# Performance work log

Hardware: AMD Instinct MI355X
Metric: run time of the kernel (lower is better)

Reference implementation:

```python
import jax, jax.numpy as jnp
import numpy as np

N = 50000        # nodes
E = 1_600_000    # edges
IN = 64          # in_feats
H = 128          # h_feats
L = 5            # num_layers
G = 512          # graphs in batch
C = 10           # num_classes


def setup_inputs() -> dict:
    key = jax.random.key(0)
    ks = jax.random.split(key, 12)
    s = 0.05
    x = jax.random.normal(ks[0], (N, IN), jnp.float32)
    edge_index = jax.random.randint(ks[1], (2, E), 0, N, dtype=jnp.int32)
    batch = jnp.sort(jax.random.randint(ks[2], (N,), 0, G, dtype=jnp.int32))
    edge_weight = jax.random.uniform(ks[3], (E,), jnp.float32)
    # GatedGraphConv params: per-layer mixing weight + shared GRUCell
    weight = jax.random.normal(ks[4], (L, H, H), jnp.float32) * s
    w_ih = jax.random.normal(ks[5], (3 * H, H), jnp.float32) * s
    w_hh = jax.random.normal(ks[6], (3 * H, H), jnp.float32) * s
    b_ih = jax.random.normal(ks[7], (3 * H,), jnp.float32) * s
    b_hh = jax.random.normal(ks[8], (3 * H,), jnp.float32) * s
    # MLP head
    dense1_w = jax.random.normal(ks[9], (4 * H, H), jnp.float32) * s
    dense1_b = jnp.zeros((4 * H,), jnp.float32)
    dense2_w = jax.random.normal(ks[10], (C, 4 * H), jnp.float32) * s
    dense2_b = jnp.zeros((C,), jnp.float32)
    return dict(x=x, edge_index=edge_index, batch=batch, edge_weight=edge_weight,
                weight=weight, w_ih=w_ih, w_hh=w_hh, b_ih=b_ih, b_hh=b_hh,
                dense1_w=dense1_w, dense1_b=dense1_b,
                dense2_w=dense2_w, dense2_b=dense2_b)


def _gru_cell(m, h, w_ih, w_hh, b_ih, b_hh):
    # torch.nn.GRUCell(input=m, hidden=h)
    gi = m @ w_ih.T + b_ih
    gh = h @ w_hh.T + b_hh
    i_r, i_z, i_n = jnp.split(gi, 3, axis=-1)
    h_r, h_z, h_n = jnp.split(gh, 3, axis=-1)
    r = jax.nn.sigmoid(i_r + h_r)
    z = jax.nn.sigmoid(i_z + h_z)
    n = jnp.tanh(i_n + r * h_n)
    return (1.0 - z) * n + z * h


def reference(x, edge_index, batch, edge_weight, weight, w_ih, w_hh, b_ih, b_hh,
              dense1_w, dense1_b, dense2_w, dense2_b):
    src, dst = edge_index[0], edge_index[1]
    # pad in_feats -> h_feats (PyG GatedGraphConv)
    h = jnp.pad(x, ((0, 0), (0, H - IN)))
    for l in range(L):
        m = h @ weight[l]                          # [N, H]
        msg = m[src] * edge_weight[:, None]        # gather + edge gating [E, H]
        agg = jax.ops.segment_sum(msg, dst, num_segments=N)  # scatter-add
        h = _gru_cell(agg, h, w_ih, w_hh, b_ih, b_hh)
    pooled = jax.ops.segment_max(h, batch, num_segments=G)   # global max pool [G, H]
    # dropout is identity in eval mode
    hid = jax.nn.relu(pooled @ dense1_w.T + dense1_b)
    out = hid @ dense2_w.T + dense2_b
    return out
```

## Files before the change

### kernel.cpp

```cpp
#include <hip/hip_runtime.h>
#include <hip/hip_bf16.h>

#define NN 50000
#define NE 1600000
#define FIN 64
#define H 128
#define NL 5
#define NG 512
#define NC 10

typedef __attribute__((ext_vector_type(8))) short short8;
typedef __attribute__((ext_vector_type(4))) float f32x4;

#define OFF_H2A   0
#define OFF_H2B   3200000
#define OFF_CUR   6400000
#define OFF_OFF   6450176
#define OFF_CSR   6500352
#define OFF_POOL  8900352
#define OFF_FWF   8965888
#define OFF_FWHH  9088768

__device__ __forceinline__ short rne_bf16(float f){
    unsigned u = __float_as_uint(f);
    unsigned r = (u + 0x7FFFu + ((u >> 16) & 1u)) >> 16;
    return (short)r;
}
__device__ __forceinline__ float bf_lo(unsigned v){ return __uint_as_float(v << 16); }
__device__ __forceinline__ float bf_hi(unsigned v){ return __uint_as_float(v & 0xFFFF0000u); }


__global__ void k_hist(const int* __restrict__ ei, int* __restrict__ cnt){
    int e = blockIdx.x*256 + threadIdx.x;
    if (e < NE) atomicAdd(&cnt[ei[NE + e]], 1);
}

__global__ void k_scan(int* __restrict__ cur, int* __restrict__ off){
    __shared__ int s[1024];
    int t = threadIdx.x;
    const int CH = 49;
    int base = t*CH;
    int m = (NN + 1) - base; if (m > CH) m = CH; if (m < 0) m = 0;
    int sum = 0;
    for (int i = 0; i < m; ++i) sum += (cur[base + i] + 15) & ~15;
    s[t] = sum; __syncthreads();
    for (int o = 1; o < 1024; o <<= 1){
        int v = (t >= o) ? s[t - o] : 0; __syncthreads();
        s[t] += v; __syncthreads();
    }
    int run = s[t] - sum;
    for (int i = 0; i < m; ++i){
        int c = (cur[base + i] + 15) & ~15;
        off[base + i] = run;
        cur[base + i] = run;
        run += c;
    }
}

__global__ void k_fill(const int* __restrict__ ei, const float* __restrict__ ew,
                       int* __restrict__ cur, unsigned* __restrict__ csr){
    int e = blockIdx.x*256 + threadIdx.x;
    if (e >= NE) return;
    int src = ei[e], dst = ei[NE + e];
    int pos = atomicAdd(&cur[dst], 1);
    csr[pos] = (unsigned)src | (((unsigned)(ushort)rne_bf16(ew[e])) << 16);
}


__global__ void k_pad(const float* __restrict__ x, ushort* __restrict__ h2a){
    int idx = blockIdx.x*256 + threadIdx.x;
    int n = idx >> 7, f = idx & 127;
    float v = (f < FIN) ? x[n*FIN + f] : 0.f;
    h2a[idx] = (ushort)rne_bf16(v);
}

__global__ void k_fuse(const float* __restrict__ W, const float* __restrict__ wih,
                       short* __restrict__ fwf){
    int idx = blockIdx.x*256 + threadIdx.x;
    int l = idx / 49152;
    int r = idx % 49152;
    int k = r / 384, n = r % 384;
    const float* wl = W + l*16384 + k*128;
    const float* wi = wih + n*128;
    float acc = 0.f;
    for (int c = 0; c < 128; ++c) acc += wl[c]*wi[c];
    int lane = ((k>>3)&3)*16 + (n&15);
    fwf[l*49152 + (((n>>4)*4 + (k>>5))*64 + lane)*8 + (k&7)] = rne_bf16(acc);
}

__global__ void k_cvt_whh(const float* __restrict__ whh, short* __restrict__ fwhh){
    int idx = blockIdx.x*256 + threadIdx.x;
    int k = idx / 384, n = idx % 384;
    float v = whh[n*128 + k];
    int lane = ((k>>3)&3)*16 + (n&15);
    fwhh[(((n>>4)*4 + (k>>5))*64 + lane)*8 + (k&7)] = rne_bf16(v);
}

__global__ void k_init_pool(unsigned* __restrict__ p){
    p[blockIdx.x*256 + threadIdx.x] = 0x007FFFFFu;
}

__global__ __launch_bounds__(256)
void k_layer(const ushort* __restrict__ h2r, ushort* __restrict__ h2w,
             const int* __restrict__ off, const unsigned* __restrict__ csr,
             const short* __restrict__ fwf, const short* __restrict__ fwhh,
             const float* __restrict__ b_ih, const float* __restrict__ b_hh,
             const int* __restrict__ batch, unsigned* __restrict__ pooled,
             int last){
    __shared__ ushort tl[16*136];
    int tid = threadIdx.x;
    int n0 = blockIdx.x * 16;
    int wave = tid >> 6, lane = tid & 63;
    int lane_lo = lane & 15, quad = lane >> 4;
    int grp = lane >> 4, fl = lane & 15;

    for (int sub = 0; sub < 4; ++sub){
        int node = n0 + wave*4 + sub;
        int start = __builtin_amdgcn_readfirstlane(off[node]);
        int end   = __builtin_amdgcn_readfirstlane(off[node + 1]);
        float a0=0.f,a1=0.f,a2=0.f,a3=0.f,a4=0.f,a5=0.f,a6=0.f,a7=0.f;
        const ushort* hb = h2r + fl*8;
        for (int i = start; i < end; i += 16){
            uint4 c = *(const uint4*)(csr + i + grp*4);
            uint4 v0 = *(const uint4*)(hb + (c.x & 0xFFFFu)*H);
            uint4 v1 = *(const uint4*)(hb + (c.y & 0xFFFFu)*H);
            uint4 v2 = *(const uint4*)(hb + (c.z & 0xFFFFu)*H);
            uint4 v3 = *(const uint4*)(hb + (c.w & 0xFFFFu)*H);
            float w0 = bf_hi(c.x), w1 = bf_hi(c.y), w2 = bf_hi(c.z), w3 = bf_hi(c.w);
            a0 += w0*bf_lo(v0.x); a1 += w0*bf_hi(v0.x); a2 += w0*bf_lo(v0.y); a3 += w0*bf_hi(v0.y);
            a4 += w0*bf_lo(v0.z); a5 += w0*bf_hi(v0.z); a6 += w0*bf_lo(v0.w); a7 += w0*bf_hi(v0.w);
            a0 += w1*bf_lo(v1.x); a1 += w1*bf_hi(v1.x); a2 += w1*bf_lo(v1.y); a3 += w1*bf_hi(v1.y);
            a4 += w1*bf_lo(v1.z); a5 += w1*bf_hi(v1.z); a6 += w1*bf_lo(v1.w); a7 += w1*bf_hi(v1.w);
            a0 += w2*bf_lo(v2.x); a1 += w2*bf_hi(v2.x); a2 += w2*bf_lo(v2.y); a3 += w2*bf_hi(v2.y);
            a4 += w2*bf_lo(v2.z); a5 += w2*bf_hi(v2.z); a6 += w2*bf_lo(v2.w); a7 += w2*bf_hi(v2.w);
            a0 += w3*bf_lo(v3.x); a1 += w3*bf_hi(v3.x); a2 += w3*bf_lo(v3.y); a3 += w3*bf_hi(v3.y);
            a4 += w3*bf_lo(v3.z); a5 += w3*bf_hi(v3.z); a6 += w3*bf_lo(v3.w); a7 += w3*bf_hi(v3.w);
        }
        a0 += __shfl_xor(a0,16); a1 += __shfl_xor(a1,16); a2 += __shfl_xor(a2,16); a3 += __shfl_xor(a3,16);
        a4 += __shfl_xor(a4,16); a5 += __shfl_xor(a5,16); a6 += __shfl_xor(a6,16); a7 += __shfl_xor(a7,16);
        a0 += __shfl_xor(a0,32); a1 += __shfl_xor(a1,32); a2 += __shfl_xor(a2,32); a3 += __shfl_xor(a3,32);
        a4 += __shfl_xor(a4,32); a5 += __shfl_xor(a5,32); a6 += __shfl_xor(a6,32); a7 += __shfl_xor(a7,32);
        if (lane < 16){
            short8 hbv;
            hbv[0]=rne_bf16(a0); hbv[1]=rne_bf16(a1); hbv[2]=rne_bf16(a2); hbv[3]=rne_bf16(a3);
            hbv[4]=rne_bf16(a4); hbv[5]=rne_bf16(a5); hbv[6]=rne_bf16(a6); hbv[7]=rne_bf16(a7);
            *(short8*)(tl + (wave*4 + sub)*136 + fl*8) = hbv;
        }
    }
    __syncthreads();

    f32x4 ai[6], ah[6];
    #pragma unroll
    for (int i = 0; i < 6; ++i){ ai[i] = (f32x4){0.f,0.f,0.f,0.f}; ah[i] = (f32x4){0.f,0.f,0.f,0.f}; }

    const ushort* arow_t = tl + lane_lo*136;
    const ushort* arow_h = h2r + (size_t)(n0 + lane_lo)*H;
    #pragma unroll
    for (int kt = 0; kt < 4; ++kt){
        short8 at  = *(const short8*)(arow_t + kt*32 + quad*8);
        short8 ahh = *(const short8*)(arow_h + kt*32 + quad*8);
        #pragma unroll
        for (int s = 0; s < 3; ++s){
            #pragma unroll
            for (int t16 = 0; t16 < 2; ++t16){
                int tile = (s*8 + wave*2 + t16)*4 + kt;
                short8 bi = *(const short8*)(fwf  + tile*512 + lane*8);
                short8 bh = *(const short8*)(fwhh + tile*512 + lane*8);
                ai[s*2+t16] = __builtin_amdgcn_mfma_f32_16x16x32_bf16(at,  bi, ai[s*2+t16], 0, 0, 0);
                ah[s*2+t16] = __builtin_amdgcn_mfma_f32_16x16x32_bf16(ahh, bh, ah[s*2+t16], 0, 0, 0);
            }
        }
    }

    #pragma unroll
    for (int t16 = 0; t16 < 2; ++t16){
        int j = wave*32 + t16*16 + lane_lo;
        float bir = b_ih[j], biz = b_ih[128 + j], bin_ = b_ih[256 + j];
        float bhr = b_hh[j], bhz = b_hh[128 + j], bhn  = b_hh[256 + j];
        #pragma unroll
        for (int r = 0; r < 4; ++r){
            int row = n0 + quad*4 + r;
            float gir = ai[t16][r]     + bir, ghr = ah[t16][r]     + bhr;
            float giz = ai[2 + t16][r] + biz, ghz = ah[2 + t16][r] + bhz;
            float gin = ai[4 + t16][r] + bin_, ghn = ah[4 + t16][r] + bhn;
            float rr = 1.f/(1.f + __expf(-(gir + ghr)));
            float zz = 1.f/(1.f + __expf(-(giz + ghz)));
            float nn = tanhf(gin + rr*ghn);
            float ho = __uint_as_float(((unsigned)h2r[(size_t)row*H + j]) << 16);
            float hv = (1.f - zz)*nn + zz*ho;
            if (!last){
                h2w[(size_t)row*H + j] = (ushort)rne_bf16(hv);
            } else {
                int g = batch[row];
                unsigned u = __float_as_uint(hv);
                u = (u & 0x80000000u) ? ~u : (u | 0x80000000u);
                atomicMax(pooled + g*H + j, u);
            }
        }
    }
}


__global__ void k_head(const unsigned* __restrict__ pooled,
                       const float* __restrict__ d1w, const float* __restrict__ d1b,
                       const float* __restrict__ d2w, const float* __restrict__ d2b,
                       float* __restrict__ out){
    __shared__ float sp[128];
    __shared__ float shid[512];
    int g = blockIdx.x, tid = threadIdx.x;
    if (tid < 128){
        unsigned u = pooled[g*H + tid];
        sp[tid] = __uint_as_float((u & 0x80000000u) ? (u ^ 0x80000000u) : ~u);
    }
    __syncthreads();
    for (int o = tid; o < 512; o += 256){
        float acc = d1b[o];
        for (int k = 0; k < H; ++k) acc += sp[k] * d1w[o*H + k];
        shid[o] = fmaxf(acc, 0.f);
    }
    __syncthreads();
    if (tid < NC){
        float acc = d2b[tid];
        for (int o = 0; o < 512; ++o) acc += shid[o] * d2w[tid*512 + o];
        out[g*NC + tid] = acc;
    }
}

extern "C" void kernel_launch(void* const* d_in, const int* in_sizes, int n_in,
                              void* d_out, int out_size, void* d_ws, size_t ws_size,
                              hipStream_t stream){
    const float* x     = (const float*)d_in[0];
    const int*   ei    = (const int*)d_in[1];
    const int*   batch = (const int*)d_in[2];
    const float* ew    = (const float*)d_in[3];
    const float* W     = (const float*)d_in[4];
    const float* wih   = (const float*)d_in[5];
    const float* whh   = (const float*)d_in[6];
    const float* bih   = (const float*)d_in[7];
    const float* bhh   = (const float*)d_in[8];
    const float* d1w   = (const float*)d_in[9];
    const float* d1b   = (const float*)d_in[10];
    const float* d2w   = (const float*)d_in[11];
    const float* d2b   = (const float*)d_in[12];
    float* out = (float*)d_out;

    float*  ws  = (float*)d_ws;
    ushort* h2a = (ushort*)(ws + OFF_H2A);
    ushort* h2b = (ushort*)(ws + OFF_H2B);
    int*    cur = (int*)(ws + OFF_CUR);
    int*    off = (int*)(ws + OFF_OFF);
    unsigned* csr = (unsigned*)(ws + OFF_CSR);
    unsigned* pooled = (unsigned*)(ws + OFF_POOL);
    short*  fwf  = (short*)(ws + OFF_FWF);
    short*  fwhh = (short*)(ws + OFF_FWHH);

    hipMemsetAsync(cur, 0, 50176*sizeof(int), stream);
    hipMemsetAsync(csr, 0, 2400000*sizeof(unsigned), stream);
    k_hist<<<6250, 256, 0, stream>>>(ei, cur);
    k_scan<<<1, 1024, 0, stream>>>(cur, off);
    k_fill<<<6250, 256, 0, stream>>>(ei, ew, cur, csr);

    k_fuse<<<960, 256, 0, stream>>>(W, wih, fwf);
    k_cvt_whh<<<192, 256, 0, stream>>>(whh, fwhh);
    k_pad<<<25000, 256, 0, stream>>>(x, h2a);
    k_init_pool<<<256, 256, 0, stream>>>(pooled);

    for (int l = 0; l < NL; ++l){
        ushort* h2r = (l & 1) ? h2b : h2a;
        ushort* h2w = (l & 1) ? h2a : h2b;
        k_layer<<<3125, 256, 0, stream>>>(h2r, h2w, off, csr,
                                          fwf + (size_t)l*49152, fwhh, bih, bhh,
                                          batch, pooled, (l == NL-1) ? 1 : 0);
    }

    k_head<<<NG, 256, 0, stream>>>(pooled, d1w, d1b, d2w, d2b, out);
}
```

Baseline: 920.5 us.

## Renumber nodes by descending in-degree to balance per-block gather work

```diff
diff --git a/kernel.cpp b/kernel.cpp
--- a/kernel.cpp
+++ b/kernel.cpp
@@ -20,6 +20,10 @@
 #define OFF_POOL  8900352
 #define OFF_FWF   8965888
 #define OFF_FWHH  9088768
+#define OFF_CNT   9113344
+#define OFF_PERM  9163344
+#define OFF_IPERM 9213344
+#define OFF_DBIN  9263344
 
 __device__ __forceinline__ short rne_bf16(float f){
     unsigned u = __float_as_uint(f);
@@ -35,14 +39,46 @@
     if (e < NE) atomicAdd(&cnt[ei[NE + e]], 1);
 }
 
-__global__ void k_scan(int* __restrict__ cur, int* __restrict__ off){
+__global__ void k_dhist(const int* __restrict__ cnt, int* __restrict__ dbin){
+    int n = blockIdx.x*256 + threadIdx.x;
+    if (n < NN) atomicAdd(&dbin[min(cnt[n], 255)], 1);
+}
+
+__global__ void k_dscan(int* __restrict__ dbin){
+    __shared__ int s[256], r2[256];
+    int t = threadIdx.x;
+    int u = 255 - t;
+    s[t] = dbin[t]; __syncthreads();
+    r2[u] = s[t]; __syncthreads();
+    for (int o = 1; o < 256; o <<= 1){
+        int v = (u >= o) ? r2[u - o] : 0; __syncthreads();
+        r2[u] += v; __syncthreads();
+    }
+    dbin[t] = r2[u] - s[t];
+}
+
+__global__ void k_dscatter(const int* __restrict__ cnt, int* __restrict__ cursor,
+                           int* __restrict__ perm, int* __restrict__ iperm){
+    int n = blockIdx.x*256 + threadIdx.x;
+    if (n >= NN) return;
+    int d = min(cnt[n], 255);
+    int pos = atomicAdd(&cursor[d], 1);
+    perm[pos] = n;
+    iperm[n] = pos;
+}
+
+__global__ void k_scan(const int* __restrict__ cnt, const int* __restrict__ perm,
+                       int* __restrict__ cur, int* __restrict__ off){
     __shared__ int s[1024];
     int t = threadIdx.x;
     const int CH = 49;
     int base = t*CH;
     int m = (NN + 1) - base; if (m > CH) m = CH; if (m < 0) m = 0;
     int sum = 0;
-    for (int i = 0; i < m; ++i) sum += (cur[base + i] + 15) & ~15;
+    for (int i = 0; i < m; ++i){
+        int nd = base + i;
+        if (nd < NN) sum += (cnt[perm[nd]] + 15) & ~15;
+    }
     s[t] = sum; __syncthreads();
     for (int o = 1; o < 1024; o <<= 1){
         int v = (t >= o) ? s[t - o] : 0; __syncthreads();
@@ -50,28 +86,32 @@
     }
     int run = s[t] - sum;
     for (int i = 0; i < m; ++i){
-        int c = (cur[base + i] + 15) & ~15;
-        off[base + i] = run;
-        cur[base + i] = run;
+        int nd = base + i;
+        int c = (nd < NN) ? ((cnt[perm[nd]] + 15) & ~15) : 0;
+        off[nd] = run;
+        cur[nd] = run;
         run += c;
     }
 }
 
 __global__ void k_fill(const int* __restrict__ ei, const float* __restrict__ ew,
+                       const int* __restrict__ iperm,
                        int* __restrict__ cur, unsigned* __restrict__ csr){
     int e = blockIdx.x*256 + threadIdx.x;
     if (e >= NE) return;
     int src = ei[e], dst = ei[NE + e];
-    int pos = atomicAdd(&cur[dst], 1);
-    csr[pos] = (unsigned)src | (((unsigned)(ushort)rne_bf16(ew[e])) << 16);
-}
-
-
-__global__ void k_pad(const float* __restrict__ x, ushort* __restrict__ h2a){
+    int r = iperm[dst];
+    int pos = atomicAdd(&cur[r], 1);
+    csr[pos] = (unsigned)iperm[src] | (((unsigned)(ushort)rne_bf16(ew[e])) << 16);
+}
+
+
+__global__ void k_pad(const float* __restrict__ x, const int* __restrict__ iperm,
+                      ushort* __restrict__ h2a){
     int idx = blockIdx.x*256 + threadIdx.x;
     int n = idx >> 7, f = idx & 127;
     float v = (f < FIN) ? x[n*FIN + f] : 0.f;
-    h2a[idx] = (ushort)rne_bf16(v);
+    h2a[iperm[n]*H + f] = (ushort)rne_bf16(v);
 }
 
 __global__ void k_fuse(const float* __restrict__ W, const float* __restrict__ wih,
@@ -105,8 +145,8 @@
              const int* __restrict__ off, const unsigned* __restrict__ csr,
              const short* __restrict__ fwf, const short* __restrict__ fwhh,
              const float* __restrict__ b_ih, const float* __restrict__ b_hh,
-             const int* __restrict__ batch, unsigned* __restrict__ pooled,
-             int last){
+             const int* __restrict__ batch, const int* __restrict__ perm,
+             unsigned* __restrict__ pooled, int last){
     __shared__ ushort tl[16*136];
     int tid = threadIdx.x;
     int n0 = blockIdx.x * 16;
@@ -191,7 +231,7 @@
             if (!last){
                 h2w[(size_t)row*H + j] = (ushort)rne_bf16(hv);
             } else {
-                int g = batch[row];
+                int g = batch[perm[row]];
                 unsigned u = __float_as_uint(hv);
                 u = (u & 0x80000000u) ? ~u : (u | 0x80000000u);
                 atomicMax(pooled + g*H + j, u);
@@ -253,16 +293,25 @@
     unsigned* pooled = (unsigned*)(ws + OFF_POOL);
     short*  fwf  = (short*)(ws + OFF_FWF);
     short*  fwhh = (short*)(ws + OFF_FWHH);
-
-    hipMemsetAsync(cur, 0, 50176*sizeof(int), stream);
+    int*    cnt  = (int*)(ws + OFF_CNT);
+    int*    perm = (int*)(ws + OFF_PERM);
+    int*    iperm= (int*)(ws + OFF_IPERM);
+    int*    dbin = (int*)(ws + OFF_DBIN);
+
+    hipMemsetAsync(cnt, 0, 50000*sizeof(int), stream);
+    hipMemsetAsync(dbin, 0, 256*sizeof(int), stream);
     hipMemsetAsync(csr, 0, 2400000*sizeof(unsigned), stream);
-    k_hist<<<6250, 256, 0, stream>>>(ei, cur);
-    k_scan<<<1, 1024, 0, stream>>>(cur, off);
-    k_fill<<<6250, 256, 0, stream>>>(ei, ew, cur, csr);
+
+    k_hist<<<6250, 256, 0, stream>>>(ei, cnt);
+    k_dhist<<<196, 256, 0, stream>>>(cnt, dbin);
+    k_dscan<<<1, 256, 0, stream>>>(dbin);
+    k_dscatter<<<196, 256, 0, stream>>>(cnt, dbin, perm, iperm);
+    k_scan<<<1, 1024, 0, stream>>>(cnt, perm, cur, off);
+    k_fill<<<6250, 256, 0, stream>>>(ei, ew, iperm, cur, csr);
 
     k_fuse<<<960, 256, 0, stream>>>(W, wih, fwf);
     k_cvt_whh<<<192, 256, 0, stream>>>(whh, fwhh);
-    k_pad<<<25000, 256, 0, stream>>>(x, h2a);
+    k_pad<<<25000, 256, 0, stream>>>(x, iperm, h2a);
     k_init_pool<<<256, 256, 0, stream>>>(pooled);
 
     for (int l = 0; l < NL; ++l){
@@ -270,7 +319,7 @@
         ushort* h2w = (l & 1) ? h2a : h2b;
         k_layer<<<3125, 256, 0, stream>>>(h2r, h2w, off, csr,
                                           fwf + (size_t)l*49152, fwhh, bih, bhh,
-                                          batch, pooled, (l == NL-1) ? 1 : 0);
+                                          batch, perm, pooled, (l == NL-1) ? 1 : 0);
     }
 
     k_head<<<NG, 256, 0, stream>>>(pooled, d1w, d1b, d2w, d2b, out);
```

Measured after the change: 1.180 ms. 1.28x slower.
